# Optimization experiments

Measured on AMD Instinct MI355X. Metric: run time of the kernel, lower is better.

The kernel has to match this reference:

```python
import jax, jax.numpy as jnp
import numpy as np

N_NODES = 100000
N_EDGES = 1600000
D = 64
EPS_NORM = 1e-9
EPS_DENOM = 1e-9


def setup_inputs() -> dict:
    key = jax.random.key(0)
    k1, k2, k3, k4, k5 = jax.random.split(key, 5)
    x = jax.random.normal(k1, (N_NODES, D), dtype=jnp.float32)
    z = jax.random.normal(k2, (N_NODES, D), dtype=jnp.float32)
    edge_index = jax.random.randint(k3, (2, N_EDGES), 0, N_NODES, dtype=jnp.int64)
    W = jax.random.normal(k4, (D, D), dtype=jnp.float32) * (1.0 / np.sqrt(D))
    b = jax.random.normal(k5, (D,), dtype=jnp.float32) * 0.01
    alpha = jnp.ones((), dtype=jnp.float32)
    bias_edge = jnp.zeros((), dtype=jnp.float32)
    return {"x": x, "edge_index": edge_index, "z": z, "W": W, "b": b,
            "alpha": alpha, "bias_edge": bias_edge}


def reference(x, edge_index, z, W, b, alpha, bias_edge):
    row, col = edge_index[0], edge_index[1]
    z_i = z[row]                      # [E, D] gather
    z_j = z[col]                      # [E, D] gather
    num = jnp.sum(z_i * z_j, axis=-1)                       # [E]
    den = jnp.maximum(jnp.linalg.norm(z_i, axis=-1) * jnp.linalg.norm(z_j, axis=-1), EPS_NORM)
    corr = num / den                                        # cosine correlation per edge
    logits = alpha * corr + bias_edge                       # [E]
    exp_logits = jnp.exp(logits - jnp.max(logits))          # global-max-stabilized exp
    denom = jax.ops.segment_sum(exp_logits, row, num_segments=N_NODES)  # [N]
    attn = exp_logits / (denom[row] + EPS_DENOM)            # edge softmax over incoming edges
    msgs = attn[:, None] * x[col]                           # [E, D]
    out = jax.ops.segment_sum(msgs, row, num_segments=N_NODES)          # [N, D]
    return out @ W.T + b                                    # Linear(in_dim, out_dim)
```

## Files before the change

### kernel.cpp

```cpp
#include <hip/hip_runtime.h>
#include <hip/hip_fp16.h>
#include <math.h>

#define NN 100000
#define NE 1600000
#define D  64
#define NBLK 391

typedef _Float16 half2v __attribute__((ext_vector_type(2)));
typedef int int2v __attribute__((ext_vector_type(2)));
typedef unsigned int uint2v __attribute__((ext_vector_type(2)));

__device__ __forceinline__ unsigned int pack_entry(int col, float ex) {
    unsigned short hb = __half_as_ushort(__float2half(ex));
    return ((unsigned int)col << 15) | (unsigned int)(hb & 0x7FFFu);
}
__device__ __forceinline__ float unpack_ex(unsigned int pk) {
    return __half2float(__ushort_as_half((unsigned short)(pk & 0x7FFFu)));
}

__device__ __forceinline__ float dot2acc(int a, unsigned int b, float c) {
#if defined(__has_builtin) && __has_builtin(__builtin_amdgcn_fdot2)
    return __builtin_amdgcn_fdot2(__builtin_bit_cast(half2v, a),
                                  __builtin_bit_cast(half2v, b), c, false);
#else
    float2 fa = __half22float2(*(const __half2*)&a);
    float2 fb = __half22float2(*(const __half2*)&b);
    return fmaf(fa.y, fb.y, fmaf(fa.x, fb.x, c));
#endif
}

__global__ __launch_bounds__(256) void k_prep_count(const float* __restrict__ z,
                                                    const float* __restrict__ x,
                                                    const float* __restrict__ W,
                                                    __half* __restrict__ zx,
                                                    const int* __restrict__ ei,
                                                    int* __restrict__ cnt8,
                                                    unsigned int* __restrict__ rankr) {
    __shared__ unsigned int WtP[32 * 64];
    {
        const float2* W2 = (const float2*)W;
        for (int i = threadIdx.x; i < 2048; i += 256) {
            int j = i >> 5, d2 = i & 31;
            float2 wp = W2[j * 32 + d2];
            half2v h;
            h.x = (_Float16)wp.x;
            h.y = (_Float16)wp.y;
            WtP[d2 * 64 + j] = __builtin_bit_cast(unsigned int, h);
        }
    }
    __syncthreads();
    const int lane = threadIdx.x & 63;
    int wave = blockIdx.x * 4 + (threadIdx.x >> 6);
    int nWaves = gridDim.x * 4;
    for (int n = wave; n < NN; n += nWaves) {
        float zv = z[n * D + lane];
        float s = zv * zv;
#pragma unroll
        for (int off = 32; off; off >>= 1) s += __shfl_xor(s, off);
        float inv = 1.0f / sqrtf(fmaxf(s, 1e-18f));
        zx[(size_t)n * 128 + lane] = __float2half(zv * inv);
        float xv = x[n * D + lane];
        float pa = __shfl(xv, 2 * (lane & 31));
        float pb = __shfl(xv, 2 * (lane & 31) + 1);
        half2v pkh;
        pkh.x = (_Float16)pa;
        pkh.y = (_Float16)pb;
        int pki = __builtin_bit_cast(int, pkh);
        float y = 0.0f;
#pragma unroll
        for (int d2 = 0; d2 < 32; ++d2) {
            int pv = __shfl(pki, d2);
            unsigned int wv = WtP[d2 * 64 + lane];
            y = dot2acc(pv, wv, y);
        }
        zx[(size_t)n * 128 + 64 + lane] = __float2half(y);
    }
    const int myc = (blockIdx.x & 7) * NN;
    const unsigned int xcdbits = (unsigned int)(blockIdx.x & 7) << 12;
    int e0 = (blockIdx.x * 256 + threadIdx.x) * 2;
    if (e0 < NE) {
        int2v rr = __builtin_nontemporal_load((const int2v*)(ei + e0));
        int rk0 = atomicAdd(&cnt8[myc + rr.x], 1);
        int rk1 = atomicAdd(&cnt8[myc + rr.y], 1);
        uint2v pk;
        pk.x = ((unsigned int)rr.x << 15) | xcdbits | (unsigned int)rk0;
        pk.y = ((unsigned int)rr.y << 15) | xcdbits | (unsigned int)rk1;
        __builtin_nontemporal_store(pk, (uint2v*)(rankr + e0));
    }
}

__global__ __launch_bounds__(256) void k_scan1(const int* __restrict__ cnt8,
                                               int* __restrict__ inc,
                                               int* __restrict__ bsum) {
    __shared__ int sh[256];
    int gid = blockIdx.x * 256 + threadIdx.x;
    int v = 0;
    if (gid < NN) {
#pragma unroll
        for (int k = 0; k < 8; ++k) v += cnt8[k * NN + gid];
    }
    sh[threadIdx.x] = v;
    __syncthreads();
    for (int off = 1; off < 256; off <<= 1) {
        int t = (threadIdx.x >= off) ? sh[threadIdx.x - off] : 0;
        __syncthreads();
        sh[threadIdx.x] += t;
        __syncthreads();
    }
    if (gid < NN) inc[gid] = sh[threadIdx.x];
    if (threadIdx.x == 255) bsum[blockIdx.x] = sh[255];
}

__global__ __launch_bounds__(512) void k_scan2(int* __restrict__ bsum) {
    __shared__ int sh[512];
    int v = (threadIdx.x < NBLK) ? bsum[threadIdx.x] : 0;
    sh[threadIdx.x] = v;
    __syncthreads();
    for (int off = 1; off < 512; off <<= 1) {
        int t = (threadIdx.x >= off) ? sh[threadIdx.x - off] : 0;
        __syncthreads();
        sh[threadIdx.x] += t;
        __syncthreads();
    }
    if (threadIdx.x < NBLK) bsum[threadIdx.x] = sh[threadIdx.x] - v;
}

__global__ __launch_bounds__(256) void k_scan3(const int* __restrict__ cnt8,
                                               const int* __restrict__ inc,
                                               const int* __restrict__ bsum,
                                               int* __restrict__ row_start,
                                               int* __restrict__ row_start8,
                                               int* __restrict__ tot) {
    int gid = blockIdx.x * 256 + threadIdx.x;
    if (gid >= NN) return;
    int c[8];
    int s8 = 0;
#pragma unroll
    for (int k = 0; k < 8; ++k) {
        c[k] = cnt8[k * NN + gid];
        s8 += c[k];
    }
    int ex = inc[gid] - s8 + bsum[blockIdx.x];
    row_start[gid] = ex;
    tot[gid] = s8;
    int base = ex;
#pragma unroll
    for (int k = 0; k < 8; ++k) {
        row_start8[k * NN + gid] = base;
        base += c[k];
    }
}

__global__ __launch_bounds__(256) void k_place(const int* __restrict__ ei,
                                               const unsigned int* __restrict__ rankr,
                                               const int* __restrict__ row_start8,
                                               int* __restrict__ colidx) {
    int e0 = (blockIdx.x * 256 + threadIdx.x) * 2;
    if (e0 >= NE) return;
    uint2v rr = __builtin_nontemporal_load((const uint2v*)(rankr + e0));
    int2v cc = __builtin_nontemporal_load((const int2v*)(ei + NE + e0));
    int r0 = (int)(rr.x >> 15), x0 = (int)((rr.x >> 12) & 7u), k0 = (int)(rr.x & 0xFFFu);
    int r1 = (int)(rr.y >> 15), x1 = (int)((rr.y >> 12) & 7u), k1 = (int)(rr.y & 0xFFFu);
    __builtin_nontemporal_store(cc.x, &colidx[row_start8[x0 * NN + r0] + k0]);
    __builtin_nontemporal_store(cc.y, &colidx[row_start8[x1 * NN + r1] + k1]);
}

__global__ __launch_bounds__(256) void k_node(const __half* __restrict__ zx,
                                              const int* __restrict__ colidx,
                                              const int* __restrict__ row_start,
                                              const int* __restrict__ tot,
                                              const float* __restrict__ b,
                                              const float* __restrict__ alpha_p,
                                              const float* __restrict__ bias_p,
                                              float* __restrict__ out) {
    const int lane = threadIdx.x & 63;
    const int sub = lane & 15;
    int w = (blockIdx.x * blockDim.x + threadIdx.x) >> 6;
    int nb = w * 4;
    int n = nb + (lane >> 4);
    const float alpha = *alpha_p;
    const float bias = *bias_p;
    const float Mest = fabsf(alpha) + bias;
    int rs = row_start[n];
    int c = tot[n];
    float bv = b[lane];
    const float4* zi4 = (const float4*)(zx + (size_t)n * 128);
    float4 zi[8];
#pragma unroll
    for (int k = 0; k < 8; ++k) zi[k] = zi4[k];
    int cmax = c;
    cmax = max(cmax, __shfl_xor(cmax, 16));
    cmax = max(cmax, __shfl_xor(cmax, 32));
    float a0A = 0.0f, a0B = 0.0f, a1A = 0.0f, a1B = 0.0f;
    float a2A = 0.0f, a2B = 0.0f, a3A = 0.0f, a3B = 0.0f;
    float dsum = 0.0f;
    for (int base = 0; base < cmax; base += 16) {
        int idx = base + sub;
        bool valid = idx < c;
        int col = valid ? colidx[rs + idx] : 0;
        const float4* zj4 = (const float4*)(zx + (size_t)col * 128);
        float4 zj[8];
#pragma unroll
        for (int k = 0; k < 8; ++k) zj[k] = zj4[k];
        float d0 = 0.0f, d1 = 0.0f, d2 = 0.0f, d3 = 0.0f;
#pragma unroll
        for (int k = 0; k < 8; ++k) {
            const int* ha = (const int*)&zi[k];
            const unsigned int* hb = (const unsigned int*)&zj[k];
            d0 = dot2acc(ha[0], hb[0], d0);
            d1 = dot2acc(ha[1], hb[1], d1);
            d2 = dot2acc(ha[2], hb[2], d2);
            d3 = dot2acc(ha[3], hb[3], d3);
        }
        float dot = (d0 + d1) + (d2 + d3);
        float ex = valid ? __expf(alpha * dot + bias - Mest) : 0.0f;
        unsigned int pk = pack_entry(col, ex);
        float t = ex;
        t += __shfl_xor(t, 1);
        t += __shfl_xor(t, 2);
        t += __shfl_xor(t, 4);
        t += __shfl_xor(t, 8);
        dsum += t;
#define PHASE_B(GG, ACCA, ACCB)                                                                    \
        {                                                                                          \
            int cg = __shfl(c, GG * 16);                                                           \
            int mg = cg - base;                                                                    \
            mg = mg > 16 ? 16 : mg;                                                               \
            int j = 0;                                                                             \
            for (; j + 4 <= mg; j += 4) {                                                          \
                unsigned int q0 = (unsigned int)__builtin_amdgcn_readlane((int)pk, GG * 16 + j);   \
                unsigned int q1 = (unsigned int)__builtin_amdgcn_readlane((int)pk, GG * 16 + j + 1); \
                unsigned int q2 = (unsigned int)__builtin_amdgcn_readlane((int)pk, GG * 16 + j + 2); \
                unsigned int q3 = (unsigned int)__builtin_amdgcn_readlane((int)pk, GG * 16 + j + 3); \
                float x0 = __half2float(zx[(size_t)(q0 >> 15) * 128 + 64 + lane]);                 \
                float x1 = __half2float(zx[(size_t)(q1 >> 15) * 128 + 64 + lane]);                 \
                float x2 = __half2float(zx[(size_t)(q2 >> 15) * 128 + 64 + lane]);                 \
                float x3 = __half2float(zx[(size_t)(q3 >> 15) * 128 + 64 + lane]);                 \
                ACCA = fmaf(unpack_ex(q0), x0, ACCA);                                              \
                ACCB = fmaf(unpack_ex(q1), x1, ACCB);                                              \
                ACCA = fmaf(unpack_ex(q2), x2, ACCA);                                              \
                ACCB = fmaf(unpack_ex(q3), x3, ACCB);                                              \
            }                                                                                      \
            for (; j < mg; ++j) {                                                                  \
                unsigned int q0 = (unsigned int)__builtin_amdgcn_readlane((int)pk, GG * 16 + j);   \
                float x0 = __half2float(zx[(size_t)(q0 >> 15) * 128 + 64 + lane]);                 \
                ACCA = fmaf(unpack_ex(q0), x0, ACCA);                                              \
            }                                                                                      \
        }
        PHASE_B(0, a0A, a0B)
        PHASE_B(1, a1A, a1B)
        PHASE_B(2, a2A, a2B)
        PHASE_B(3, a3A, a3B)
#undef PHASE_B
    }
    float dg0 = __shfl(dsum, 0);
    float dg1 = __shfl(dsum, 16);
    float dg2 = __shfl(dsum, 32);
    float dg3 = __shfl(dsum, 48);
    out[(size_t)(nb + 0) * D + lane] = (a0A + a0B) / (dg0 + 1e-9f) + bv;
    out[(size_t)(nb + 1) * D + lane] = (a1A + a1B) / (dg1 + 1e-9f) + bv;
    out[(size_t)(nb + 2) * D + lane] = (a2A + a2B) / (dg2 + 1e-9f) + bv;
    out[(size_t)(nb + 3) * D + lane] = (a3A + a3B) / (dg3 + 1e-9f) + bv;
}

extern "C" void kernel_launch(void* const* d_in, const int* in_sizes, int n_in,
                              void* d_out, int out_size, void* d_ws, size_t ws_size,
                              hipStream_t stream) {
    const float* x = (const float*)d_in[0];
    const int* ei = (const int*)d_in[1];
    const float* z = (const float*)d_in[2];
    const float* W = (const float*)d_in[3];
    const float* b = (const float*)d_in[4];
    const float* alpha = (const float*)d_in[5];
    const float* bias_edge = (const float*)d_in[6];
    float* out = (float*)d_out;

    char* ws = (char*)d_ws;
    size_t off = 0;
    __half* zx = (__half*)(ws + off); off += (size_t)NN * 128 * 2;
    int* colidx = (int*)(ws + off); off += (size_t)NE * 4;
    unsigned int* rankr = (unsigned int*)(ws + off); off += (size_t)NE * 4;
    int* cnt8 = (int*)(ws + off); off += (size_t)8 * NN * 4;
    int* row_start8 = (int*)(ws + off); off += (size_t)8 * NN * 4;
    int* inc = (int*)(ws + off); off += (size_t)NN * 4;
    int* row_start = (int*)(ws + off); off += (size_t)NN * 4;
    int* tot = (int*)(ws + off); off += (size_t)NN * 4;
    int* bsum = (int*)(ws + off); off += 512 * 4;

    hipMemsetAsync(cnt8, 0, (size_t)8 * NN * 4, stream);
    k_prep_count<<<4096, 256, 0, stream>>>(z, x, W, zx, ei, cnt8, rankr);
    k_scan1<<<NBLK, 256, 0, stream>>>(cnt8, inc, bsum);
    k_scan2<<<1, 512, 0, stream>>>(bsum);
    k_scan3<<<NBLK, 256, 0, stream>>>(cnt8, inc, bsum, row_start, row_start8, tot);
    k_place<<<(NE / 2 + 255) / 256, 256, 0, stream>>>(ei, rankr, row_start8, colidx);
    k_node<<<NN / 16, 256, 0, stream>>>(zx, colidx, row_start, tot, b, alpha, bias_edge, out);
}
```

Measured before the change: 233.5 us.

## Fuse three scan kernels into one using a grid-wide spin barrier

Result: slower. 267.9 us (+14.7%).

```diff
diff --git a/kernel.cpp b/kernel.cpp
--- a/kernel.cpp
+++ b/kernel.cpp
@@ -6,6 +6,7 @@
 #define NE 1600000
 #define D  64
 #define NBLK 391
+#define AGG_COUNTER 400
 
 typedef _Float16 half2v __attribute__((ext_vector_type(2)));
 typedef int int2v __attribute__((ext_vector_type(2)));
@@ -37,6 +38,13 @@
                                                     const int* __restrict__ ei,
                                                     int* __restrict__ cnt8,
                                                     unsigned int* __restrict__ rankr) {
+    const int myc = (blockIdx.x & 7) * NN;
+    const unsigned int xcdbits = (unsigned int)(blockIdx.x & 7) << 12;
+    int e0 = (blockIdx.x * 256 + threadIdx.x) * 2;
+    bool havec = e0 < NE;
+    int2v rr;
+    if (havec) rr = __builtin_nontemporal_load((const int2v*)(ei + e0));
+
     __shared__ unsigned int WtP[32 * 64];
     {
         const float2* W2 = (const float2*)W;
@@ -50,6 +58,13 @@
         }
     }
     __syncthreads();
+
+    int rk0 = 0, rk1 = 0;
+    if (havec) {
+        rk0 = atomicAdd(&cnt8[myc + rr.x], 1);
+        rk1 = atomicAdd(&cnt8[myc + rr.y], 1);
+    }
+
     const int lane = threadIdx.x & 63;
     int wave = blockIdx.x * 4 + (threadIdx.x >> 6);
     int nWaves = gridDim.x * 4;
@@ -76,13 +91,8 @@
         }
         zx[(size_t)n * 128 + 64 + lane] = __float2half(y);
     }
-    const int myc = (blockIdx.x & 7) * NN;
-    const unsigned int xcdbits = (unsigned int)(blockIdx.x & 7) << 12;
-    int e0 = (blockIdx.x * 256 + threadIdx.x) * 2;
-    if (e0 < NE) {
-        int2v rr = __builtin_nontemporal_load((const int2v*)(ei + e0));
-        int rk0 = atomicAdd(&cnt8[myc + rr.x], 1);
-        int rk1 = atomicAdd(&cnt8[myc + rr.y], 1);
+
+    if (havec) {
         uint2v pk;
         pk.x = ((unsigned int)rr.x << 15) | xcdbits | (unsigned int)rk0;
         pk.y = ((unsigned int)rr.y << 15) | xcdbits | (unsigned int)rk1;
@@ -90,58 +100,54 @@
     }
 }
 
-__global__ __launch_bounds__(256) void k_scan1(const int* __restrict__ cnt8,
-                                               int* __restrict__ inc,
-                                               int* __restrict__ bsum) {
+__global__ __launch_bounds__(256) void k_scan(const int* __restrict__ cnt8,
+                                              int* __restrict__ agg,
+                                              int* __restrict__ row_start,
+                                              int* __restrict__ row_start8,
+                                              int* __restrict__ tot) {
     __shared__ int sh[256];
-    int gid = blockIdx.x * 256 + threadIdx.x;
-    int v = 0;
+    const int tid = threadIdx.x;
+    const int bid = blockIdx.x;
+    int gid = bid * 256 + tid;
+    int c[8];
+    int s8 = 0;
     if (gid < NN) {
 #pragma unroll
-        for (int k = 0; k < 8; ++k) v += cnt8[k * NN + gid];
-    }
-    sh[threadIdx.x] = v;
+        for (int k = 0; k < 8; ++k) {
+            c[k] = cnt8[k * NN + gid];
+            s8 += c[k];
+        }
+    }
+    sh[tid] = s8;
     __syncthreads();
     for (int off = 1; off < 256; off <<= 1) {
-        int t = (threadIdx.x >= off) ? sh[threadIdx.x - off] : 0;
+        int t = (tid >= off) ? sh[tid - off] : 0;
         __syncthreads();
-        sh[threadIdx.x] += t;
+        sh[tid] += t;
         __syncthreads();
     }
-    if (gid < NN) inc[gid] = sh[threadIdx.x];
-    if (threadIdx.x == 255) bsum[blockIdx.x] = sh[255];
-}
-
-__global__ __launch_bounds__(512) void k_scan2(int* __restrict__ bsum) {
-    __shared__ int sh[512];
-    int v = (threadIdx.x < NBLK) ? bsum[threadIdx.x] : 0;
-    sh[threadIdx.x] = v;
+    int incl = sh[tid];
+    if (tid == 255) {
+        __hip_atomic_store(&agg[bid], incl, __ATOMIC_RELEASE, __HIP_MEMORY_SCOPE_AGENT);
+        __hip_atomic_fetch_add(&agg[AGG_COUNTER], 1, __ATOMIC_RELEASE, __HIP_MEMORY_SCOPE_AGENT);
+    }
+    if (tid == 0) {
+        while (__hip_atomic_load(&agg[AGG_COUNTER], __ATOMIC_ACQUIRE, __HIP_MEMORY_SCOPE_AGENT) < NBLK) {
+        }
+    }
     __syncthreads();
-    for (int off = 1; off < 512; off <<= 1) {
-        int t = (threadIdx.x >= off) ? sh[threadIdx.x - off] : 0;
+    int mysum = 0;
+    for (int j = tid; j < bid; j += 256)
+        mysum += __hip_atomic_load(&agg[j], __ATOMIC_RELAXED, __HIP_MEMORY_SCOPE_AGENT);
+    sh[tid] = mysum;
+    __syncthreads();
+    for (int off = 128; off; off >>= 1) {
+        if (tid < off) sh[tid] += sh[tid + off];
         __syncthreads();
-        sh[threadIdx.x] += t;
-        __syncthreads();
-    }
-    if (threadIdx.x < NBLK) bsum[threadIdx.x] = sh[threadIdx.x] - v;
-}
-
-__global__ __launch_bounds__(256) void k_scan3(const int* __restrict__ cnt8,
-                                               const int* __restrict__ inc,
-                                               const int* __restrict__ bsum,
-                                               int* __restrict__ row_start,
-                                               int* __restrict__ row_start8,
-                                               int* __restrict__ tot) {
-    int gid = blockIdx.x * 256 + threadIdx.x;
+    }
+    int bbase = sh[0];
     if (gid >= NN) return;
-    int c[8];
-    int s8 = 0;
-#pragma unroll
-    for (int k = 0; k < 8; ++k) {
-        c[k] = cnt8[k * NN + gid];
-        s8 += c[k];
-    }
-    int ex = inc[gid] - s8 + bsum[blockIdx.x];
+    int ex = bbase + incl - s8;
     row_start[gid] = ex;
     tot[gid] = s8;
     int base = ex;
@@ -282,17 +288,14 @@
     int* colidx = (int*)(ws + off); off += (size_t)NE * 4;
     unsigned int* rankr = (unsigned int*)(ws + off); off += (size_t)NE * 4;
     int* cnt8 = (int*)(ws + off); off += (size_t)8 * NN * 4;
+    int* agg = (int*)(ws + off); off += 512 * 4;
     int* row_start8 = (int*)(ws + off); off += (size_t)8 * NN * 4;
-    int* inc = (int*)(ws + off); off += (size_t)NN * 4;
     int* row_start = (int*)(ws + off); off += (size_t)NN * 4;
     int* tot = (int*)(ws + off); off += (size_t)NN * 4;
-    int* bsum = (int*)(ws + off); off += 512 * 4;
-
-    hipMemsetAsync(cnt8, 0, (size_t)8 * NN * 4, stream);
+
+    hipMemsetAsync(cnt8, 0, (size_t)8 * NN * 4 + 512 * 4, stream);
     k_prep_count<<<4096, 256, 0, stream>>>(z, x, W, zx, ei, cnt8, rankr);
-    k_scan1<<<NBLK, 256, 0, stream>>>(cnt8, inc, bsum);
-    k_scan2<<<1, 512, 0, stream>>>(bsum);
-    k_scan3<<<NBLK, 256, 0, stream>>>(cnt8, inc, bsum, row_start, row_start8, tot);
+    k_scan<<<NBLK, 256, 0, stream>>>(cnt8, agg, row_start, row_start8, tot);
     k_place<<<(NE / 2 + 255) / 256, 256, 0, stream>>>(ei, rankr, row_start8, colidx);
     k_node<<<NN / 16, 256, 0, stream>>>(zx, colidx, row_start, tot, b, alpha, bias_edge, out);
 }
```
